# Kernel optimization log

Hardware: AMD Instinct MI355X
Metric: run time of the kernel (lower is better)

The kernel has to match this reference:

```python
import jax, jax.numpy as jnp
import numpy as np
import math

B, SES, SEQ, H, K = 16, 16, 64, 512, 32
L = SES * SEQ


def setup_inputs() -> dict:
    key = jax.random.key(0)
    ks = jax.random.split(key, 16)
    s = 1.0 / math.sqrt(H)
    return {
        "user_emb": jax.random.normal(ks[0], (B, H), jnp.float32),
        "item_emb": jax.random.normal(ks[1], (B, SES, SEQ, H), jnp.float32),
        "mask": jnp.zeros((B, L, K), jnp.float32),
        "index": jax.random.randint(ks[2], (L, K), 0, L, jnp.int64),
        "Wq": jax.random.normal(ks[3], (H, H), jnp.float32) * s,
        "bq": jnp.zeros((H,), jnp.float32),
        "Wk": jax.random.normal(ks[4], (H, H), jnp.float32) * s,
        "bk": jnp.zeros((H,), jnp.float32),
        "Wv": jax.random.normal(ks[5], (H, H), jnp.float32) * s,
        "bv": jnp.zeros((H,), jnp.float32),
        "Wd": jax.random.normal(ks[6], (H, H), jnp.float32) * s,
        "bd": jnp.zeros((H,), jnp.float32),
        "ln_g": jnp.ones((H,), jnp.float32),
        "ln_b": jnp.zeros((H,), jnp.float32),
    }


def reference(user_emb, item_emb, mask, index, Wq, bq, Wk, bk, Wv, bv, Wd, bd, ln_g, ln_b):
    b, ses, seq, h = item_emb.shape
    l = ses * seq
    item_flat = item_emb.reshape(b, l, h)
    q = user_emb @ Wq.T + bq                       # [B, H]
    k = item_flat @ Wk.T + bk                      # [B, L, H]
    v = item_flat @ Wv.T + bv                      # [B, L, H]
    # scalar query against all L keys, scaled by sqrt(hidden_size)
    scores = jnp.einsum("bh,blh->bl", q, k) / math.sqrt(h)
    scores = scores[:, index] + mask               # gather -> [B, L, K]
    w = jax.nn.softmax(scores, axis=-1)            # [B, L, K]
    vg = v[:, index, :]                            # gather -> [B, L, K, H]
    attn_out = jnp.einsum("blk,blkh->blh", w, vg)  # [B, L, H]
    dense = attn_out @ Wd.T + bd
    x = dense + item_flat                          # residual (dropout = identity, eval)
    mu = jnp.mean(x, axis=-1, keepdims=True)
    var = jnp.var(x, axis=-1, keepdims=True)
    y = (x - mu) / jnp.sqrt(var + 1e-12) * ln_g + ln_b
    return y.reshape(b, ses, seq, h)
```

## Files before the change

kernel.cpp:

```cpp
#include <hip/hip_runtime.h>
#include <math.h>

constexpr int HD   = 512;
constexpr int LL   = 1024;
constexpr int MT   = 16384;
constexpr int KNBR = 32;
constexpr float SCL = 0.04419417382415922f;

typedef __attribute__((ext_vector_type(8))) short  bf16x8;
typedef __attribute__((ext_vector_type(4))) float  f32x4;

__device__ inline float b2f(unsigned short u) {
    union { unsigned int i; float f; } v; v.i = (unsigned int)u << 16; return v.f;
}
__device__ inline float b2f_lo(unsigned int u) {
    union { unsigned int i; float f; } v; v.i = u << 16; return v.f;
}
__device__ inline float b2f_hi(unsigned int u) {
    union { unsigned int i; float f; } v; v.i = u & 0xffff0000u; return v.f;
}
__device__ inline unsigned short f2b(float x) {
    union { float f; unsigned int u; } v; v.f = x;
    unsigned int r = v.u + 0x7fff + ((v.u >> 16) & 1);
    return (unsigned short)(r >> 16);
}

constexpr int PB_CONV_I = 8192;
constexpr int PB_CONV_W = 512;
constexpr int PB_Q      = 2048;

__global__ __launch_bounds__(256) void prep(
    const float* __restrict__ item, const float* __restrict__ Wv,
    const float* __restrict__ Wd, const float* __restrict__ u,
    const float* __restrict__ Wq, const float* __restrict__ bq,
    unsigned short* __restrict__ item_bf, unsigned short* __restrict__ item_kt,
    unsigned short* __restrict__ Wv_bf, unsigned short* __restrict__ Wd_bf,
    float* __restrict__ q)
{
    const int blk = blockIdx.x, tid = threadIdx.x;

    if (blk < PB_CONV_I) {
        const int i = blk * 1024 + tid * 4;
        float4 v = *(const float4*)&item[i];
        ushort4 o;
        o.x = f2b(v.x); o.y = f2b(v.y); o.z = f2b(v.z); o.w = f2b(v.w);
        *(ushort4*)&item_bf[i] = o;
        const int m = i >> 9, k = i & 511;
        *(ushort4*)&item_kt[((size_t)(k >> 5) * MT + m) * 32 + (k & 31)] = o;
        return;
    }
    if (blk < PB_CONV_I + PB_CONV_W) {
        const int n = HD*HD;
        const int i = (blk - PB_CONV_I) * 1024 + tid * 4;
        const float* s; unsigned short* d; int off;
        if (i < n) { s = Wv; d = Wv_bf; off = i; }
        else       { s = Wd; d = Wd_bf; off = i - n; }
        float4 v = *(const float4*)&s[off];
        ushort4 o;
        o.x = f2b(v.x); o.y = f2b(v.y); o.z = f2b(v.z); o.w = f2b(v.w);
        const int nr = off >> 9, k = off & 511;
        *(ushort4*)&d[((k >> 5) * 512 + nr) * 32 + (k & 31)] = o;
        return;
    }
    {
        const int wid  = (blk - PB_CONV_I - PB_CONV_W) * 4 + (tid >> 6);
        const int lane = tid & 63;
        const int b = wid >> 9, h = wid & 511;
        const float* ur = &u[b*HD + lane*8];
        const float* wr = &Wq[(size_t)h*HD + lane*8];
        const float4 u0 = *(const float4*)ur, u1 = *(const float4*)(ur+4);
        const float4 w0 = *(const float4*)wr, w1 = *(const float4*)(wr+4);
        float acc = u0.x*w0.x + u0.y*w0.y + u0.z*w0.z + u0.w*w0.w
                  + u1.x*w1.x + u1.y*w1.y + u1.z*w1.z + u1.w*w1.w;
        #pragma unroll
        for (int off = 32; off; off >>= 1) acc += __shfl_down(acc, off);
        if (lane == 0) q[b*HD + h] = acc + bq[h];
    }
}

__global__ __launch_bounds__(256) void gemm_v_r(
    const unsigned short* __restrict__ Akt, const unsigned short* __restrict__ Wt,
    const float* __restrict__ bv, const float* __restrict__ Wk,
    const float* __restrict__ bk, const float* __restrict__ q,
    unsigned short* __restrict__ v_bf, float* __restrict__ rbuf,
    float* __restrict__ s0buf)
{
    __shared__ unsigned short As[4][128 * 32];
    __shared__ unsigned short Bs[4][128 * 32];

    const int blk = blockIdx.x;
    const int tid = threadIdx.x;

    if (blk >= 512) {
        if (blk < 640) {
            __shared__ float red[4][64];
            const int rblk = blk - 512;
            const int b = rblk >> 3, c0 = (rblk & 7) * 64;
            const int cl = tid & 63, hg = tid >> 6;
            const float* qb = &q[b*HD];
            const float* wb = &Wk[(size_t)hg*128*HD + c0 + cl];
            float acc = 0.f;
            #pragma unroll 8
            for (int h = 0; h < 128; h++)
                acc += qb[hg*128 + h] * wb[(size_t)h*HD];
            red[hg][cl] = acc;
            __syncthreads();
            if (tid < 64)
                rbuf[b*HD + c0 + tid] = SCL *
                    (red[0][tid] + red[1][tid] + red[2][tid] + red[3][tid]);
        } else {
            __shared__ float sp[4];
            const int b = blk - 640;
            float p = q[b*HD + tid]*bk[tid] + q[b*HD + tid + 256]*bk[tid + 256];
            #pragma unroll
            for (int off = 32; off; off >>= 1) p += __shfl_down(p, off);
            if ((tid & 63) == 0) sp[tid >> 6] = p;
            __syncthreads();
            if (tid == 0) s0buf[b] = (sp[0] + sp[1] + sp[2] + sp[3]) * SCL;
        }
        return;
    }

    const int rowb = (blk & 7) | ((blk >> 5) << 3);
    const int colb = (blk >> 3) & 3;
    const int row0 = rowb * 128;
    const int col0 = colb * 128;

    const int wave = tid >> 6, lane = tid & 63;
    const int wm = (wave >> 1) * 64;
    const int wn = (wave & 1)  * 64;

    const int lrr = lane >> 2;
    const int cc  = lane & 3;
    int st_row[2], st_gchunk[2];
    #pragma unroll
    for (int t = 0; t < 2; t++) {
        const int m = wave*32 + t*16 + lrr;
        st_row[t]    = m;
        st_gchunk[t] = cc ^ ((m >> 1) & 3);
    }

    const int fr   = lane & 15;
    const int quad = lane >> 4;

    f32x4 acc[4][4];
    #pragma unroll
    for (int i = 0; i < 4; i++)
        #pragma unroll
        for (int j = 0; j < 4; j++)
            acc[i][j] = (f32x4){0.f, 0.f, 0.f, 0.f};

    int a_off[4], b_off[4];
    #pragma unroll
    for (int i = 0; i < 4; i++) {
        const int m = wm + i*16 + fr;
        a_off[i] = m*32 + ((quad ^ ((m >> 1) & 3)) << 3);
        const int n = wn + i*16 + fr;
        b_off[i] = n*32 + ((quad ^ ((n >> 1) & 3)) << 3);
    }

    auto stage = [&](int kt) {
        const int bf = kt & 3;
        #pragma unroll
        for (int t = 0; t < 2; t++) {
            const int m = st_row[t];
            const unsigned short* ga =
                &Akt[((size_t)kt*MT + row0 + m)*32 + st_gchunk[t]*8];
            __builtin_amdgcn_global_load_lds(
                (const __attribute__((address_space(1))) void*)ga,
                (__attribute__((address_space(3))) void*)&As[bf][(wave*32 + t*16)*32],
                16, 0, 0);
            const unsigned short* gw =
                &Wt[((size_t)kt*512 + col0 + m)*32 + st_gchunk[t]*8];
            __builtin_amdgcn_global_load_lds(
                (const __attribute__((address_space(1))) void*)gw,
                (__attribute__((address_space(3))) void*)&Bs[bf][(wave*32 + t*16)*32],
                16, 0, 0);
        }
    };

    auto kstep = [&](int cur, int kt_next) {
        __builtin_amdgcn_s_barrier();
        asm volatile("" ::: "memory");
        bf16x8 af[4], bfr[4];
        #pragma unroll
        for (int i = 0; i < 4; i++) {
            af[i]  = *(const bf16x8*)&As[cur][a_off[i]];
            bfr[i] = *(const bf16x8*)&Bs[cur][b_off[i]];
        }
        asm volatile("s_waitcnt lgkmcnt(0)" ::: "memory");
        __builtin_amdgcn_sched_barrier(0);
        __builtin_amdgcn_s_barrier();
        if (kt_next >= 0) stage(kt_next);
        __builtin_amdgcn_s_setprio(1);
        #pragma unroll
        for (int i = 0; i < 4; i++)
            #pragma unroll
            for (int j = 0; j < 4; j++)
                acc[i][j] = __builtin_amdgcn_mfma_f32_16x16x32_bf16(
                    af[i], bfr[j], acc[i][j], 0, 0, 0);
        __builtin_amdgcn_s_setprio(0);
    };

    stage(0); stage(1); stage(2); stage(3);

    for (int s = 0; s <= 12; ++s) {
        asm volatile("s_waitcnt vmcnt(12)" ::: "memory");
        kstep(s & 3, (s + 4 <= 15) ? s + 4 : -1);
    }
    asm volatile("s_waitcnt vmcnt(8)" ::: "memory");  kstep(1, -1);
    asm volatile("s_waitcnt vmcnt(4)" ::: "memory");  kstep(2, -1);
    asm volatile("s_waitcnt vmcnt(0)" ::: "memory");  kstep(3, -1);

    #pragma unroll
    for (int j = 0; j < 4; j++) {
        const int col = col0 + wn + j*16 + fr;
        const float bb = bv[col];
        #pragma unroll
        for (int i = 0; i < 4; i++) {
            #pragma unroll
            for (int r = 0; r < 4; r++) {
                const int row = row0 + wm + i*16 + quad*4 + r;
                v_bf[(size_t)row*HD + col] = f2b(acc[i][j][r] + bb);
            }
        }
    }
}

__global__ __launch_bounds__(256) void gp_scores(
    const float* __restrict__ rbuf, const float* __restrict__ s0buf,
    const unsigned short* __restrict__ item_bf, float* __restrict__ scores)
{
    const int m = blockIdx.x * 4 + (threadIdx.x >> 6);
    const int lane = threadIdx.x & 63;
    const int b = m >> 10;
    const unsigned short* ir = &item_bf[(size_t)m*HD + lane*8];
    const uint4 iv = *(const uint4*)ir;
    const float* rr = &rbuf[b*HD + lane*8];
    const float4 r0 = *(const float4*)rr;
    const float4 r1 = *(const float4*)(rr + 4);
    float acc = r0.x*b2f_lo(iv.x) + r0.y*b2f_hi(iv.x)
              + r0.z*b2f_lo(iv.y) + r0.w*b2f_hi(iv.y)
              + r1.x*b2f_lo(iv.z) + r1.y*b2f_hi(iv.z)
              + r1.z*b2f_lo(iv.w) + r1.w*b2f_hi(iv.w);
    #pragma unroll
    for (int off = 32; off; off >>= 1) acc += __shfl_down(acc, off);
    if (lane == 0) scores[m] = acc + s0buf[b];
}

__global__ __launch_bounds__(256) void dense_attn_ln(
    const float* __restrict__ scores, const int* __restrict__ index,
    const float* __restrict__ mask, const unsigned short* __restrict__ v,
    const unsigned short* __restrict__ Wt,
    const float* __restrict__ bd, const unsigned short* __restrict__ res,
    const float* __restrict__ ln_g, const float* __restrict__ ln_b,
    float* __restrict__ out)
{
    __shared__ unsigned short att[32 * 528];
    __shared__ float rsum[4][32], rsq[4][32];

    const int tid  = threadIdx.x;
    const int wave = tid >> 6, lane = tid & 63;
    const int bid  = blockIdx.x;
    const int rblk = (bid & 7) * 64 + (bid >> 3);
    const int row0 = rblk * 32;
    const int b    = row0 >> 10;

    const int fr = lane & 15, quad = lane >> 4;

    const unsigned short* wbase = Wt + ((size_t)wave*128 + fr)*32 + quad*8;
    auto loadW = [&](int kt, bf16x8* dst) {
        #pragma unroll
        for (int j = 0; j < 8; j++)
            dst[j] = *(const bf16x8*)(wbase + (size_t)kt*512*32 + j*16*32);
    };

    bf16x8 wreg[2][8];
    loadW(0, wreg[0]);
    loadW(1, wreg[1]);

    {
        const unsigned short* vb = v + (size_t)b * LL * HD;
        const int loff = lane * 8;
        const int t = lane & 31;
        for (int rr = 0; rr < 8; ++rr) {
            const int lrow = wave * 8 + rr;
            const int m = row0 + lrow;
            const int l = m & 1023;

            const int idx = index[l*KNBR + t];
            const float s = scores[b*LL + idx] + mask[(size_t)m*KNBR + t];

            float mx = s;
            #pragma unroll
            for (int off = 16; off; off >>= 1) mx = fmaxf(mx, __shfl_xor(mx, off));
            const float e = __expf(s - mx);
            float sum = e;
            #pragma unroll
            for (int off = 16; off; off >>= 1) sum += __shfl_xor(sum, off);
            const float w = e / sum;

            float a[8] = {};
            #pragma unroll 8
            for (int t2 = 0; t2 < KNBR; t2++) {
                const int   it = __builtin_amdgcn_readlane(idx, t2);
                const float wt = __int_as_float(
                    __builtin_amdgcn_readlane(__float_as_int(w), t2));
                const uint4 pv = *(const uint4*)(vb + (size_t)it*HD + loff);
                a[0] += wt * b2f_lo(pv.x); a[1] += wt * b2f_hi(pv.x);
                a[2] += wt * b2f_lo(pv.y); a[3] += wt * b2f_hi(pv.y);
                a[4] += wt * b2f_lo(pv.z); a[5] += wt * b2f_hi(pv.z);
                a[6] += wt * b2f_lo(pv.w); a[7] += wt * b2f_hi(pv.w);
            }
            uint4 o;
            o.x = (unsigned int)f2b(a[0]) | ((unsigned int)f2b(a[1]) << 16);
            o.y = (unsigned int)f2b(a[2]) | ((unsigned int)f2b(a[3]) << 16);
            o.z = (unsigned int)f2b(a[4]) | ((unsigned int)f2b(a[5]) << 16);
            o.w = (unsigned int)f2b(a[6]) | ((unsigned int)f2b(a[7]) << 16);
            const int byteoff = lrow*1040 + ((lane*16) ^ ((lrow & 7) << 4));
            *(uint4*)((char*)att + byteoff) = o;
        }
    }
    __syncthreads();

    f32x4 acc[2][8];
    #pragma unroll
    for (int i = 0; i < 2; i++)
        #pragma unroll
        for (int j = 0; j < 8; j++)
            acc[i][j] = (f32x4){0.f, 0.f, 0.f, 0.f};

    int a_row[2];
    #pragma unroll
    for (int i = 0; i < 2; i++) a_row[i] = i*16 + fr;

    #pragma unroll
    for (int s = 0; s < 16; ++s) {
        bf16x8 af[2];
        #pragma unroll
        for (int i = 0; i < 2; i++) {
            const int cb = (s*64 + quad*16) ^ ((a_row[i] & 7) << 4);
            af[i] = *(const bf16x8*)((const char*)att + a_row[i]*1040 + cb);
        }
        bf16x8 cur[8];
        #pragma unroll
        for (int j = 0; j < 8; j++) cur[j] = wreg[s & 1][j];
        #pragma unroll
        for (int i = 0; i < 2; i++)
            #pragma unroll
            for (int j = 0; j < 8; j++)
                acc[i][j] = __builtin_amdgcn_mfma_f32_16x16x32_bf16(
                    af[i], cur[j], acc[i][j], 0, 0, 0);
        if (s + 2 < 16) loadW(s + 2, wreg[s & 1]);
    }
    __syncthreads();

    unsigned short* rs = att;
    #pragma unroll
    for (int u2 = 0; u2 < 8; u2++) {
        const int id = tid*8 + u2;
        const int rr = id >> 6, c8 = id & 63;
        *(uint4*)&rs[rr*528 + c8*8] =
            *(const uint4*)&res[(size_t)(row0 + rr)*HD + c8*8];
    }
    __syncthreads();

    float bdv[8], gv[8], lbv[8];
    #pragma unroll
    for (int j = 0; j < 8; j++) {
        const int col = wave*128 + j*16 + fr;
        bdv[j] = bd[col]; gv[j] = ln_g[col]; lbv[j] = ln_b[col];
    }

    #pragma unroll
    for (int i = 0; i < 2; i++) {
        #pragma unroll
        for (int r = 0; r < 4; r++) {
            const int lrow = i*16 + quad*4 + r;
            float a1 = 0.f, a2 = 0.f;
            #pragma unroll
            for (int j = 0; j < 8; j++) {
                const int col = wave*128 + j*16 + fr;
                float val = acc[i][j][r] + bdv[j] + b2f(rs[lrow*528 + col]);
                acc[i][j][r] = val;
                a1 += val; a2 += val*val;
            }
            #pragma unroll
            for (int off = 1; off < 16; off <<= 1) {
                a1 += __shfl_xor(a1, off);
                a2 += __shfl_xor(a2, off);
            }
            if (fr == 0) { rsum[wave][lrow] = a1; rsq[wave][lrow] = a2; }
        }
    }
    __syncthreads();

    #pragma unroll
    for (int i = 0; i < 2; i++) {
        #pragma unroll
        for (int r = 0; r < 4; r++) {
            const int lrow = i*16 + quad*4 + r;
            const float tot  = rsum[0][lrow] + rsum[1][lrow]
                             + rsum[2][lrow] + rsum[3][lrow];
            const float tot2 = rsq[0][lrow]  + rsq[1][lrow]
                             + rsq[2][lrow]  + rsq[3][lrow];
            const float mu  = tot * (1.f/HD);
            const float var = tot2 * (1.f/HD) - mu*mu;
            const float inv = rsqrtf(var + 1e-12f);
            const size_t gr = (size_t)(row0 + lrow) * HD;
            #pragma unroll
            for (int j = 0; j < 8; j++) {
                const int col = wave*128 + j*16 + fr;
                out[gr + col] = (acc[i][j][r] - mu)*inv*gv[j] + lbv[j];
            }
        }
    }
}

extern "C" void kernel_launch(void* const* d_in, const int* in_sizes, int n_in,
                              void* d_out, int out_size, void* d_ws, size_t ws_size,
                              hipStream_t stream) {
    const float* user_emb = (const float*)d_in[0];
    const float* item_emb = (const float*)d_in[1];
    const float* mask     = (const float*)d_in[2];
    const int*   index    = (const int*)  d_in[3];
    const float* Wq = (const float*)d_in[4];  const float* bq = (const float*)d_in[5];
    const float* Wk = (const float*)d_in[6];  const float* bk = (const float*)d_in[7];
    const float* Wv = (const float*)d_in[8];  const float* bv = (const float*)d_in[9];
    const float* Wd = (const float*)d_in[10]; const float* bd = (const float*)d_in[11];
    const float* ln_g = (const float*)d_in[12];
    const float* ln_b = (const float*)d_in[13];

    float* out = (float*)d_out;

    char* p = (char*)d_ws;
    unsigned short* item_bf = (unsigned short*)p; p += (size_t)MT*HD*2;
    unsigned short* item_kt = (unsigned short*)p; p += (size_t)MT*HD*2;
    unsigned short* v_bf    = (unsigned short*)p; p += (size_t)MT*HD*2;
    unsigned short* Wv_bf   = (unsigned short*)p; p += (size_t)HD*HD*2;
    unsigned short* Wd_bf   = (unsigned short*)p; p += (size_t)HD*HD*2;
    float* q      = (float*)p; p += 16*HD*4;
    float* rbuf   = (float*)p; p += 16*HD*4;
    float* s0buf  = (float*)p; p += 16*4;
    float* scores = (float*)p; p += MT*4;

    prep<<<PB_CONV_I + PB_CONV_W + PB_Q, 256, 0, stream>>>(
        item_emb, Wv, Wd, user_emb, Wq, bq,
        item_bf, item_kt, Wv_bf, Wd_bf, q);

    gemm_v_r<<<656, 256, 0, stream>>>(item_kt, Wv_bf, bv, Wk, bk, q,
                                      v_bf, rbuf, s0buf);

    gp_scores<<<MT/4, 256, 0, stream>>>(rbuf, s0buf, item_bf, scores);

    dense_attn_ln<<<512, 256, 0, stream>>>(scores, index, mask, v_bf,
                                           Wd_bf, bd, item_bf,
                                           ln_g, ln_b, out);
}
```

Measured before the change: 190.9 us.

## Halve GEMM LDS buffering and widen fused attention kernel to 512 threads

The V-projection GEMM drops from a 4-deep to a 2-deep LDS ring, halving its shared memory, which may allow more resident blocks but leaves less load-latency hiding. The fused attention/dense/layernorm kernel now runs 8 waves per block instead of 4. Each wave handles half the output columns and half the gathered rows, which cuts per-thread register use for accumulators and W fragments. The LayerNorm reduction is extended to eight partial sums, and the launch and launch bounds are updated to match.

```diff
diff --git a/kernel.cpp b/kernel.cpp
--- a/kernel.cpp
+++ b/kernel.cpp
@@ -85,8 +85,8 @@
     unsigned short* __restrict__ v_bf, float* __restrict__ rbuf,
     float* __restrict__ s0buf)
 {
-    __shared__ unsigned short As[4][128 * 32];
-    __shared__ unsigned short Bs[4][128 * 32];
+    __shared__ unsigned short As[2][128 * 32];
+    __shared__ unsigned short Bs[2][128 * 32];
 
     const int blk = blockIdx.x;
     const int tid = threadIdx.x;
@@ -159,8 +159,7 @@
         b_off[i] = n*32 + ((quad ^ ((n >> 1) & 3)) << 3);
     }
 
-    auto stage = [&](int kt) {
-        const int bf = kt & 3;
+    auto stage = [&](int bf, int kt) {
         #pragma unroll
         for (int t = 0; t < 2; t++) {
             const int m = st_row[t];
@@ -179,9 +178,15 @@
         }
     };
 
-    auto kstep = [&](int cur, int kt_next) {
+    stage(0, 0);
+    stage(1, 1);
+
+    for (int s = 0; s < 15; ++s) {
+        asm volatile("s_waitcnt vmcnt(4)" ::: "memory");
         __builtin_amdgcn_s_barrier();
         asm volatile("" ::: "memory");
+
+        const int cur = s & 1;
         bf16x8 af[4], bfr[4];
         #pragma unroll
         for (int i = 0; i < 4; i++) {
@@ -191,7 +196,9 @@
         asm volatile("s_waitcnt lgkmcnt(0)" ::: "memory");
         __builtin_amdgcn_sched_barrier(0);
         __builtin_amdgcn_s_barrier();
-        if (kt_next >= 0) stage(kt_next);
+
+        if (s + 2 < 16) stage(cur, s + 2);
+
         __builtin_amdgcn_s_setprio(1);
         #pragma unroll
         for (int i = 0; i < 4; i++)
@@ -200,17 +207,26 @@
                 acc[i][j] = __builtin_amdgcn_mfma_f32_16x16x32_bf16(
                     af[i], bfr[j], acc[i][j], 0, 0, 0);
         __builtin_amdgcn_s_setprio(0);
-    };
-
-    stage(0); stage(1); stage(2); stage(3);
-
-    for (int s = 0; s <= 12; ++s) {
-        asm volatile("s_waitcnt vmcnt(12)" ::: "memory");
-        kstep(s & 3, (s + 4 <= 15) ? s + 4 : -1);
-    }
-    asm volatile("s_waitcnt vmcnt(8)" ::: "memory");  kstep(1, -1);
-    asm volatile("s_waitcnt vmcnt(4)" ::: "memory");  kstep(2, -1);
-    asm volatile("s_waitcnt vmcnt(0)" ::: "memory");  kstep(3, -1);
+    }
+    {
+        asm volatile("s_waitcnt vmcnt(0)" ::: "memory");
+        __builtin_amdgcn_s_barrier();
+        asm volatile("" ::: "memory");
+        bf16x8 af[4], bfr[4];
+        #pragma unroll
+        for (int i = 0; i < 4; i++) {
+            af[i]  = *(const bf16x8*)&As[1][a_off[i]];
+            bfr[i] = *(const bf16x8*)&Bs[1][b_off[i]];
+        }
+        asm volatile("s_waitcnt lgkmcnt(0)" ::: "memory");
+        __builtin_amdgcn_sched_barrier(0);
+        #pragma unroll
+        for (int i = 0; i < 4; i++)
+            #pragma unroll
+            for (int j = 0; j < 4; j++)
+                acc[i][j] = __builtin_amdgcn_mfma_f32_16x16x32_bf16(
+                    af[i], bfr[j], acc[i][j], 0, 0, 0);
+    }
 
     #pragma unroll
     for (int j = 0; j < 4; j++) {
@@ -248,7 +264,7 @@
     if (lane == 0) scores[m] = acc + s0buf[b];
 }
 
-__global__ __launch_bounds__(256) void dense_attn_ln(
+__global__ __launch_bounds__(512, 4) void dense_attn_ln(
     const float* __restrict__ scores, const int* __restrict__ index,
     const float* __restrict__ mask, const unsigned short* __restrict__ v,
     const unsigned short* __restrict__ Wt,
@@ -257,7 +273,7 @@
     float* __restrict__ out)
 {
     __shared__ unsigned short att[32 * 528];
-    __shared__ float rsum[4][32], rsq[4][32];
+    __shared__ float rsum[8][32], rsq[8][32];
 
     const int tid  = threadIdx.x;
     const int wave = tid >> 6, lane = tid & 63;
@@ -268,14 +284,14 @@
 
     const int fr = lane & 15, quad = lane >> 4;
 
-    const unsigned short* wbase = Wt + ((size_t)wave*128 + fr)*32 + quad*8;
+    const unsigned short* wbase = Wt + ((size_t)wave*64 + fr)*32 + quad*8;
     auto loadW = [&](int kt, bf16x8* dst) {
         #pragma unroll
-        for (int j = 0; j < 8; j++)
+        for (int j = 0; j < 4; j++)
             dst[j] = *(const bf16x8*)(wbase + (size_t)kt*512*32 + j*16*32);
     };
 
-    bf16x8 wreg[2][8];
+    bf16x8 wreg[2][4];
     loadW(0, wreg[0]);
     loadW(1, wreg[1]);
 
@@ -283,8 +299,8 @@
         const unsigned short* vb = v + (size_t)b * LL * HD;
         const int loff = lane * 8;
         const int t = lane & 31;
-        for (int rr = 0; rr < 8; ++rr) {
-            const int lrow = wave * 8 + rr;
+        for (int rr = 0; rr < 4; ++rr) {
+            const int lrow = wave * 4 + rr;
             const int m = row0 + lrow;
             const int l = m & 1023;
 
@@ -323,11 +339,11 @@
     }
     __syncthreads();
 
-    f32x4 acc[2][8];
+    f32x4 acc[2][4];
     #pragma unroll
     for (int i = 0; i < 2; i++)
         #pragma unroll
-        for (int j = 0; j < 8; j++)
+        for (int j = 0; j < 4; j++)
             acc[i][j] = (f32x4){0.f, 0.f, 0.f, 0.f};
 
     int a_row[2];
@@ -342,13 +358,13 @@
             const int cb = (s*64 + quad*16) ^ ((a_row[i] & 7) << 4);
             af[i] = *(const bf16x8*)((const char*)att + a_row[i]*1040 + cb);
         }
-        bf16x8 cur[8];
-        #pragma unroll
-        for (int j = 0; j < 8; j++) cur[j] = wreg[s & 1][j];
+        bf16x8 cur[4];
+        #pragma unroll
+        for (int j = 0; j < 4; j++) cur[j] = wreg[s & 1][j];
         #pragma unroll
         for (int i = 0; i < 2; i++)
             #pragma unroll
-            for (int j = 0; j < 8; j++)
+            for (int j = 0; j < 4; j++)
                 acc[i][j] = __builtin_amdgcn_mfma_f32_16x16x32_bf16(
                     af[i], cur[j], acc[i][j], 0, 0, 0);
         if (s + 2 < 16) loadW(s + 2, wreg[s & 1]);
@@ -357,18 +373,18 @@
 
     unsigned short* rs = att;
     #pragma unroll
-    for (int u2 = 0; u2 < 8; u2++) {
-        const int id = tid*8 + u2;
+    for (int u2 = 0; u2 < 4; u2++) {
+        const int id = tid*4 + u2;
         const int rr = id >> 6, c8 = id & 63;
         *(uint4*)&rs[rr*528 + c8*8] =
             *(const uint4*)&res[(size_t)(row0 + rr)*HD + c8*8];
     }
     __syncthreads();
 
-    float bdv[8], gv[8], lbv[8];
-    #pragma unroll
-    for (int j = 0; j < 8; j++) {
-        const int col = wave*128 + j*16 + fr;
+    float bdv[4], gv[4], lbv[4];
+    #pragma unroll
+    for (int j = 0; j < 4; j++) {
+        const int col = wave*64 + j*16 + fr;
         bdv[j] = bd[col]; gv[j] = ln_g[col]; lbv[j] = ln_b[col];
     }
 
@@ -379,8 +395,8 @@
             const int lrow = i*16 + quad*4 + r;
             float a1 = 0.f, a2 = 0.f;
             #pragma unroll
-            for (int j = 0; j < 8; j++) {
-                const int col = wave*128 + j*16 + fr;
+            for (int j = 0; j < 4; j++) {
+                const int col = wave*64 + j*16 + fr;
                 float val = acc[i][j][r] + bdv[j] + b2f(rs[lrow*528 + col]);
                 acc[i][j][r] = val;
                 a1 += val; a2 += val*val;
@@ -400,17 +416,19 @@
         #pragma unroll
         for (int r = 0; r < 4; r++) {
             const int lrow = i*16 + quad*4 + r;
-            const float tot  = rsum[0][lrow] + rsum[1][lrow]
-                             + rsum[2][lrow] + rsum[3][lrow];
-            const float tot2 = rsq[0][lrow]  + rsq[1][lrow]
-                             + rsq[2][lrow]  + rsq[3][lrow];
+            float tot = 0.f, tot2 = 0.f;
+            #pragma unroll
+            for (int w2 = 0; w2 < 8; w2++) {
+                tot  += rsum[w2][lrow];
+                tot2 += rsq[w2][lrow];
+            }
             const float mu  = tot * (1.f/HD);
             const float var = tot2 * (1.f/HD) - mu*mu;
             const float inv = rsqrtf(var + 1e-12f);
             const size_t gr = (size_t)(row0 + lrow) * HD;
             #pragma unroll
-            for (int j = 0; j < 8; j++) {
-                const int col = wave*128 + j*16 + fr;
+            for (int j = 0; j < 4; j++) {
+                const int col = wave*64 + j*16 + fr;
                 out[gr + col] = (acc[i][j][r] - mu)*inv*gv[j] + lbv[j];
             }
         }
@@ -453,7 +471,7 @@
 
     gp_scores<<<MT/4, 256, 0, stream>>>(rbuf, s0buf, item_bf, scores);
 
-    dense_attn_ln<<<512, 256, 0, stream>>>(scores, index, mask, v_bf,
+    dense_attn_ln<<<512, 512, 0, stream>>>(scores, index, mask, v_bf,
                                            Wd_bf, bd, item_bf,
                                            ln_g, ln_b, out);
 }
```

After: 179.7 us. 1.06x faster.
